# Optimization experiments

Hardware: AMD Instinct MI355X
Metric: run time of the kernel (lower is better)

Reference implementation:

```python
import jax, jax.numpy as jnp
import numpy as np

N = 100000     # graph nodes
D = 256        # input_dim
E = 1600000    # edges (avg degree 16)
S = 512        # sentences in the (single) doc
EMAX = 8       # max entities per sentence
H = 256        # lstm hidden_dim
ODIM = 1       # output_dim
NCONV = 2
EPS = 1e-6


def setup_inputs() -> dict:
    key = jax.random.key(0)
    ks = jax.random.split(key, 12)
    sc = 1.0 / np.sqrt(D)
    return {
        "x": jax.random.normal(ks[0], (N, D), jnp.float32),
        "edge_index": jax.random.randint(ks[1], (2, E), 0, N, jnp.int32),
        "entity_idx": jax.random.randint(ks[2], (S, EMAX), 0, N, jnp.int32),
        "entity_mask": jax.random.randint(ks[3], (S, EMAX), 0, 2, jnp.int32),
        "nsp_scores": jax.random.uniform(ks[4], (1, S - 1), jnp.float32),
        "cls_tokens": jax.random.normal(ks[5], (1, D), jnp.float32),
        "conv_W": jax.random.normal(ks[6], (NCONV, D, D), jnp.float32) * sc,
        "sent_W": jax.random.normal(ks[7], (D, D), jnp.float32) * sc,
        "sent_b": jnp.zeros((D,), jnp.float32),
        "W_ih": jax.random.normal(ks[8], (4 * H, D), jnp.float32) * sc,
        "W_hh": jax.random.normal(ks[9], (4 * H, H), jnp.float32) * sc,
        "b_ih": jnp.zeros((4 * H,), jnp.float32),
        "b_hh": jnp.zeros((4 * H,), jnp.float32),
        "red_W": jax.random.normal(ks[10], (256, D), jnp.float32) * sc,
        "red_b": jnp.zeros((256,), jnp.float32),
        "fin_W": jax.random.normal(ks[11], (ODIM, 512), jnp.float32) * (1.0 / np.sqrt(512.0)),
        "fin_b": jnp.full((ODIM,), 0.1, jnp.float32),
    }


def _forward(x, nsp_scores, cls_tokens, conv_W, sent_W, sent_b,
             W_ih, W_hh, b_ih, b_hh, red_W, red_b, fin_W, fin_b,
             edge_index, entity_idx, entity_mask):
    src, dst = edge_index[0], edge_index[1]
    # degree normalization: norm_e = deg[dst]^-1/2 * deg[src]^-1/2
    deg = jax.ops.segment_sum(jnp.ones((E,), x.dtype), dst, num_segments=N)
    dis = jnp.where(deg > 0, deg ** -0.5, jnp.zeros((), x.dtype))
    norm = dis[dst] * dis[src]                           # [E]
    h = x
    for i in range(NCONV):                               # GCN: transform, gather, weight, scatter-add
        msg = norm[:, None] * (h @ conv_W[i])[src]       # [E, D]
        h = jax.nn.relu(jax.ops.segment_sum(msg, dst, num_segments=N))
    # per-sentence entity gather -> linear+relu -> masked sum / (eps + count)
    ent = h[entity_idx]                                  # [S, EMAX, D]
    mask = entity_mask.astype(h.dtype)                   # [S, EMAX]
    lin = jax.nn.relu(ent @ sent_W.T + sent_b)           # [S, EMAX, D]
    sums = (lin * mask[..., None]).sum(axis=1)           # [S, D]
    lengths = mask.sum(axis=1)                           # [S]
    sent_feat = sums / (EPS + lengths)[:, None]          # [S, D]
    # single-layer unidirectional LSTM over sentences (batch = 1 doc); pytorch gate order i,f,g,o
    def step(carry, xt):
        h_t, c_t = carry
        gates = xt @ W_ih.T + b_ih + h_t @ W_hh.T + b_hh  # [1, 4H]
        i_, f_, g_, o_ = jnp.split(gates, 4, axis=-1)
        c = jax.nn.sigmoid(f_) * c_t + jax.nn.sigmoid(i_) * jnp.tanh(g_)
        hn = jax.nn.sigmoid(o_) * jnp.tanh(c)
        return (hn, c), hn
    h0 = jnp.zeros((1, H), x.dtype)
    c0 = jnp.zeros((1, H), x.dtype)
    _, outs = jax.lax.scan(step, (h0, c0), sent_feat[:, None, :])  # outs: [S, 1, H]
    output = jnp.swapaxes(outs, 0, 1)                    # [1, S, H]
    # NSP-score-weighted sum over adjacent lstm outputs
    sol = (nsp_scores[..., None] * (output[:, :-1] + output[:, 1:])).sum(axis=1)  # [1, H]
    red = cls_tokens[0] @ red_W.T + red_b                # [256]
    comb = jnp.concatenate([sol[0], red], axis=0)        # [512]
    out = comb @ fin_W.T + fin_b                         # [ODIM]
    return jax.nn.sigmoid(jax.nn.relu(out))


def reference(x, edge_index, entity_idx, entity_mask, nsp_scores, cls_tokens,
              conv_W, sent_W, sent_b, W_ih, W_hh, b_ih, b_hh,
              red_W, red_b, fin_W, fin_b):
    return _forward(x, nsp_scores, cls_tokens, conv_W, sent_W, sent_b,
                    W_ih, W_hh, b_ih, b_hh, red_W, red_b, fin_W, fin_b,
                    edge_index, entity_idx, entity_mask)
```

## Files before the change

kernel.cpp:

```cpp
#include <hip/hip_runtime.h>
#include <hip/hip_fp16.h>
#include <stdint.h>

constexpr int N    = 100000;
constexpr int D    = 256;
constexpr int E    = 1600000;
constexpr int S    = 512;
constexpr int EMAX = 8;
constexpr int H    = 256;
constexpr int G4   = 4 * H;
constexpr int NB   = (N + 255) / 256;

typedef _Float16 h2_t __attribute__((ext_vector_type(2)));
typedef __attribute__((ext_vector_type(8))) short short8;
typedef __attribute__((ext_vector_type(4))) float f32x4;

static __device__ __forceinline__ float fdot2f(uint32_t a, uint32_t b, float c) {
#if __has_builtin(__builtin_amdgcn_fdot2)
    return __builtin_amdgcn_fdot2(__builtin_bit_cast(h2_t, a), __builtin_bit_cast(h2_t, b), c, false);
#else
    __half2 ha = __builtin_bit_cast(__half2, a), hb = __builtin_bit_cast(__half2, b);
    float2 fa = __half22float2(ha), fb = __half22float2(hb);
    return c + fa.x * fb.x + fa.y * fb.y;
#endif
}

static __device__ __forceinline__ uint32_t bf16rne(float f) {
    uint32_t u = __builtin_bit_cast(uint32_t, f);
    return (u + 0x7FFFu + ((u >> 16) & 1u)) >> 16;
}
static __device__ __forceinline__ uint32_t pk2(float a, float b) {
    return bf16rne(a) | (bf16rne(b) << 16);
}
static __device__ __forceinline__ float bf2f(uint32_t hi16) {
    return __builtin_bit_cast(float, hi16 << 16);
}
static __device__ __forceinline__ float sigm(float x) { return 1.f / (1.f + __expf(-x)); }
static __device__ __forceinline__ float tanhfast(float x) {
    float e = __expf(-2.f * x);
    return 2.f / (1.f + e) - 1.f;
}

__global__ void k_deg(const int* __restrict__ dst, int* __restrict__ deg) {
    int e = blockIdx.x * 256 + threadIdx.x;
    if (e < E) atomicAdd(&deg[dst[e]], 1);
}

__global__ void k_dis(const int* __restrict__ deg, float* __restrict__ dis) {
    int n = blockIdx.x * 256 + threadIdx.x;
    if (n < N) {
        int d = deg[n];
        dis[n] = (d > 0) ? (1.0f / sqrtf((float)d)) : 0.0f;
    }
}

__global__ void k_scan1(const int* __restrict__ deg, int* __restrict__ bsum) {
    __shared__ int s[256];
    int i = blockIdx.x * 256 + threadIdx.x;
    s[threadIdx.x] = (i < N) ? deg[i] : 0;
    __syncthreads();
    for (int off = 128; off > 0; off >>= 1) {
        if (threadIdx.x < off) s[threadIdx.x] += s[threadIdx.x + off];
        __syncthreads();
    }
    if (threadIdx.x == 0) bsum[blockIdx.x] = s[0];
}

__global__ void k_scan2(const int* __restrict__ bsum, int* __restrict__ boff, int* __restrict__ row_ptr) {
    __shared__ int s[512];
    int t = threadIdx.x;
    int v = (t < NB) ? bsum[t] : 0;
    s[t] = v;
    __syncthreads();
    for (int off = 1; off < 512; off <<= 1) {
        int u = (t >= off) ? s[t - off] : 0;
        __syncthreads();
        s[t] += u;
        __syncthreads();
    }
    if (t < NB) boff[t] = s[t] - v;
    if (t == NB - 1) row_ptr[N] = s[t];
}

__global__ void k_scan3(const int* __restrict__ deg, const int* __restrict__ boff, int* __restrict__ row_ptr) {
    __shared__ int s[256];
    int t = threadIdx.x, i = blockIdx.x * 256 + t;
    int v = (i < N) ? deg[i] : 0;
    s[t] = v;
    __syncthreads();
    for (int off = 1; off < 256; off <<= 1) {
        int u = (t >= off) ? s[t - off] : 0;
        __syncthreads();
        s[t] += u;
        __syncthreads();
    }
    if (i < N) row_ptr[i] = boff[blockIdx.x] + s[t] - v;
}

__global__ void k_fill(const int* __restrict__ src, const int* __restrict__ dst,
                       const float* __restrict__ dis, const int* __restrict__ row_ptr,
                       int* __restrict__ cnt, int* __restrict__ col, float* __restrict__ ew) {
    int e = blockIdx.x * 256 + threadIdx.x;
    if (e < E) {
        int s_ = src[e], d_ = dst[e];
        float w = dis[d_] * dis[s_];
        int p = row_ptr[d_] + atomicAdd(&cnt[d_], 1);
        col[p] = s_;
        ew[p]  = w;
    }
}

__global__ void k_cvtB(const float* __restrict__ W, ushort* __restrict__ Bt) {
    int i = blockIdx.x * 256 + threadIdx.x;
    if (i < 2 * 256 * 256) {
        int L = i >> 16, n = (i >> 8) & 255, k = i & 255;
        Bt[i] = (ushort)bf16rne(W[L * 65536 + k * 256 + n]);
    }
}

template<bool AF32>
__global__ __launch_bounds__(512) void k_mmb(const void* __restrict__ Av, const ushort* __restrict__ Bt,
                                             ushort* __restrict__ Cb, int M) {
    __shared__ ushort As[128 * 32];
    __shared__ ushort Bs[256 * 32];
    const float*  Af = (const float*)Av;
    const ushort* Ah = (const ushort*)Av;
    int tid = threadIdx.x;
    int lane = tid & 63;
    int wid = tid >> 6, wr = wid >> 2, wc = wid & 3;
    int m0 = blockIdx.x * 128;
    int ra = tid >> 2, ca = tid & 3;

    f32x4 acc[4][4];
#pragma unroll
    for (int mi = 0; mi < 4; mi++)
#pragma unroll
        for (int ni = 0; ni < 4; ni++) acc[mi][ni] = (f32x4){0.f, 0.f, 0.f, 0.f};

    auto ldA = [&](int kt) -> uint4 {
        uint4 r{0u, 0u, 0u, 0u};
        int grow = m0 + ra;
        if (grow < M) {
            if constexpr (AF32) {
                const float* ap = Af + (size_t)grow * 256 + kt * 32 + ca * 8;
                float4 f0 = *(const float4*)ap;
                float4 f1 = *(const float4*)(ap + 4);
                r.x = pk2(f0.x, f0.y); r.y = pk2(f0.z, f0.w);
                r.z = pk2(f1.x, f1.y); r.w = pk2(f1.z, f1.w);
            } else {
                r = *(const uint4*)(Ah + (size_t)grow * 256 + kt * 32 + ca * 8);
            }
        }
        return r;
    };

    uint4 pa  = ldA(0);
    uint4 pb0 = *(const uint4*)&Bt[(size_t)ra * 256 + ca * 8];
    uint4 pb1 = *(const uint4*)&Bt[(size_t)(ra + 128) * 256 + ca * 8];

    for (int kt = 0; kt < 8; kt++) {
        *(uint4*)&As[ra * 32 + ca * 8] = pa;
        *(uint4*)&Bs[ra * 32 + ca * 8] = pb0;
        *(uint4*)&Bs[(ra + 128) * 32 + ca * 8] = pb1;
        __syncthreads();
        if (kt < 7) {
            pa  = ldA(kt + 1);
            pb0 = *(const uint4*)&Bt[(size_t)ra * 256 + (kt + 1) * 32 + ca * 8];
            pb1 = *(const uint4*)&Bt[(size_t)(ra + 128) * 256 + (kt + 1) * 32 + ca * 8];
        }
        short8 af[4], bf[4];
#pragma unroll
        for (int mi = 0; mi < 4; mi++)
            af[mi] = __builtin_bit_cast(short8,
                *(const uint4*)&As[(wr * 64 + mi * 16 + (lane & 15)) * 32 + (lane >> 4) * 8]);
#pragma unroll
        for (int ni = 0; ni < 4; ni++)
            bf[ni] = __builtin_bit_cast(short8,
                *(const uint4*)&Bs[(wc * 64 + ni * 16 + (lane & 15)) * 32 + (lane >> 4) * 8]);
#pragma unroll
        for (int mi = 0; mi < 4; mi++)
#pragma unroll
            for (int ni = 0; ni < 4; ni++)
                acc[mi][ni] = __builtin_amdgcn_mfma_f32_16x16x32_bf16(af[mi], bf[ni], acc[mi][ni], 0, 0, 0);
        __syncthreads();
    }

#pragma unroll
    for (int mi = 0; mi < 4; mi++)
#pragma unroll
        for (int j = 0; j < 4; j++) {
            int row = m0 + wr * 64 + mi * 16 + (lane >> 4) * 4 + j;
            if (row < M) {
#pragma unroll
                for (int ni = 0; ni < 4; ni++) {
                    int colc = wc * 64 + ni * 16 + (lane & 15);
                    Cb[(size_t)row * 256 + colc] = (ushort)bf16rne(acc[mi][ni][j]);
                }
            }
        }
}

__global__ __launch_bounds__(256) void k_aggb(const ushort* __restrict__ tb, const int* __restrict__ row_ptr,
                                              const int* __restrict__ col, const float* __restrict__ ew,
                                              ushort* __restrict__ ob) {
    int wid = blockIdx.x * 4 + (threadIdx.x >> 6);
    int lane = threadIdx.x & 63;
    if (wid >= N) return;
    int beg = row_ptr[wid], end = row_ptr[wid + 1];
    float a0 = 0.f, a1 = 0.f, a2 = 0.f, a3 = 0.f;
    int e = beg;
    for (; e + 4 <= end; e += 4) {
        int s0 = col[e], s1 = col[e + 1], s2 = col[e + 2], s3 = col[e + 3];
        float w0 = ew[e], w1 = ew[e + 1], w2 = ew[e + 2], w3 = ew[e + 3];
        ushort4 v0 = *(const ushort4*)&tb[(size_t)s0 * 256 + lane * 4];
        ushort4 v1 = *(const ushort4*)&tb[(size_t)s1 * 256 + lane * 4];
        ushort4 v2 = *(const ushort4*)&tb[(size_t)s2 * 256 + lane * 4];
        ushort4 v3 = *(const ushort4*)&tb[(size_t)s3 * 256 + lane * 4];
        a0 += w0 * bf2f(v0.x) + w1 * bf2f(v1.x) + w2 * bf2f(v2.x) + w3 * bf2f(v3.x);
        a1 += w0 * bf2f(v0.y) + w1 * bf2f(v1.y) + w2 * bf2f(v2.y) + w3 * bf2f(v3.y);
        a2 += w0 * bf2f(v0.z) + w1 * bf2f(v1.z) + w2 * bf2f(v2.z) + w3 * bf2f(v3.z);
        a3 += w0 * bf2f(v0.w) + w1 * bf2f(v1.w) + w2 * bf2f(v2.w) + w3 * bf2f(v3.w);
    }
    for (; e < end; e++) {
        int s0 = col[e];
        float w0 = ew[e];
        ushort4 v0 = *(const ushort4*)&tb[(size_t)s0 * 256 + lane * 4];
        a0 += w0 * bf2f(v0.x);
        a1 += w0 * bf2f(v0.y);
        a2 += w0 * bf2f(v0.z);
        a3 += w0 * bf2f(v0.w);
    }
    a0 = fmaxf(a0, 0.f); a1 = fmaxf(a1, 0.f); a2 = fmaxf(a2, 0.f); a3 = fmaxf(a3, 0.f);
    ushort4 o = {(ushort)bf16rne(a0), (ushort)bf16rne(a1), (ushort)bf16rne(a2), (ushort)bf16rne(a3)};
    *(ushort4*)&ob[(size_t)wid * 256 + lane * 4] = o;
}

__global__ __launch_bounds__(256) void k_sent3(const ushort* __restrict__ tb, const int* __restrict__ rowp,
                                               const int* __restrict__ col, const float* __restrict__ ew,
                                               const int* __restrict__ eidx, const int* __restrict__ emask,
                                               const float* __restrict__ sW, const float* __restrict__ sb,
                                               float* __restrict__ sf) {
    __shared__ float entS[8][256];
    int s_ = blockIdx.x, tid = threadIdx.x;
#pragma unroll
    for (int e = 0; e < EMAX; e++) {
        int mk = emask[s_ * EMAX + e];
        float acc = 0.f;
        if (mk) {
            int idx = eidx[s_ * EMAX + e];
            int beg = rowp[idx], end = rowp[idx + 1];
            int ed = beg;
            for (; ed + 2 <= end; ed += 2) {
                int n0 = col[ed], n1 = col[ed + 1];
                float w0 = ew[ed], w1 = ew[ed + 1];
                acc += w0 * bf2f(tb[(size_t)n0 * 256 + tid])
                     + w1 * bf2f(tb[(size_t)n1 * 256 + tid]);
            }
            if (ed < end) {
                acc += ew[ed] * bf2f(tb[(size_t)col[ed] * 256 + tid]);
            }
        }
        entS[e][tid] = fmaxf(acc, 0.f);
    }
    __syncthreads();
    float b = sb[tid];
    float acc[8];
#pragma unroll
    for (int e = 0; e < EMAX; e++) acc[e] = b;
    for (int k4 = 0; k4 < 64; k4++) {
        float4 w = *(const float4*)&sW[(size_t)tid * 256 + k4 * 4];
#pragma unroll
        for (int e = 0; e < EMAX; e++) {
            float4 v = *(const float4*)&entS[e][k4 * 4];
            acc[e] += w.x * v.x + w.y * v.y + w.z * v.z + w.w * v.w;
        }
    }
    float sum = 0.f, len = 0.f;
#pragma unroll
    for (int e = 0; e < EMAX; e++) {
        int mk = emask[s_ * EMAX + e];
        if (mk) { sum += fmaxf(acc[e], 0.f); len += 1.f; }
    }
    sf[(size_t)s_ * 256 + tid] = sum / (1e-6f + len);
}

__global__ __launch_bounds__(256) void k_xg2(const float* __restrict__ sf, const float* __restrict__ Wih,
                                             const float* __restrict__ bih, const float* __restrict__ bhh,
                                             float* __restrict__ Xg4) {
    __shared__ float sfS[16 * 256];
    int sb = blockIdx.x, y = blockIdx.y, tid = threadIdx.x;
    for (int i = tid; i < 16 * 256; i += 256) sfS[i] = sf[(size_t)(sb * 16) * 256 + i];
    __syncthreads();
    int r = y * 256 + tid;
    float acc[16];
#pragma unroll
    for (int si = 0; si < 16; si++) acc[si] = 0.f;
    for (int k4 = 0; k4 < 64; k4++) {
        float4 w = *(const float4*)&Wih[(size_t)r * 256 + k4 * 4];
#pragma unroll
        for (int si = 0; si < 16; si++) {
            float4 v = *(const float4*)&sfS[si * 256 + k4 * 4];
            acc[si] += w.x * v.x + w.y * v.y + w.z * v.z + w.w * v.w;
        }
    }
    float bb = bih[r] + bhh[r];
#pragma unroll
    for (int si = 0; si < 16; si++)
        Xg4[(size_t)(sb * 16 + si) * 1024 + tid * 4 + y] = acc[si] + bb;
}

__global__ void k_pack(const float* __restrict__ W, uint32_t* __restrict__ Wpk) {
    int idx = blockIdx.x * 256 + threadIdx.x;
    if (idx >= 2 * 64 * 1024) return;
    int p    = idx >> 16;
    int j4   = (idx >> 12) & 15;
    int tid  = (idx >> 2) & 1023;
    int m    = idx & 3;
    int j    = j4 * 4 + m;
    int gate = (p == 0) ? ((j < 32) ? 0 : 1) : ((j < 32) ? 2 : 3);
    int jj   = j & 31;
    int q    = tid >> 8, hidx = tid & 255;
    int row  = gate * 256 + hidx;
    int c0   = q * 64 + jj * 2;
    float a = W[row * 256 + c0], b = W[row * 256 + c0 + 1];
    uint32_t lo = (uint32_t)__half_as_ushort(__float2half(a));
    uint32_t hi = (uint32_t)__half_as_ushort(__float2half(b));
    Wpk[idx] = lo | (hi << 16);
}

__global__ __launch_bounds__(1024, 4) void k_lstm4(const float* __restrict__ Xg4,
                                                   const uint32_t* __restrict__ Wpk,
                                                   const float* __restrict__ nsp,
                                                   float* __restrict__ sol_out) {
    __shared__ uint32_t gW[32768];
    __shared__ uint32_t hqd[128];
    __shared__ float4   gsm4[1024];
    __shared__ float    nspS[512];
    int tid = threadIdx.x;
    int q = tid >> 8;
    const uint4* Wpk4 = (const uint4*)Wpk;
    uint4* gW4 = (uint4*)gW;

    uint4 wr[16];
#pragma unroll
    for (int j4 = 0; j4 < 16; j4++) wr[j4] = Wpk4[j4 * 1024 + tid];
#pragma unroll
    for (int k = 0; k < 8; k++) gW4[k * 1024 + tid] = Wpk4[16384 + k * 1024 + tid];

    if (tid < 128) hqd[tid] = 0u;
    if (tid < 512) nspS[tid] = (tid < 511) ? nsp[tid] : 0.f;
    float c = 0.f, sol = 0.f;
    __syncthreads();

    for (int t = 0; t < S; t++) {
        float4 xg;
        if (tid < 256) xg = *(const float4*)&Xg4[t * 1024 + tid * 4];
        float pi = 0.f, pf = 0.f, pg = 0.f, po = 0.f;
#pragma unroll
        for (int k = 0; k < 8; k++) {
            uint4 so = Wpk4[16384 + (k + 8) * 1024 + tid];
            uint4 sg = gW4[k * 1024 + tid];
            uint4 hv = *(const uint4*)&hqd[q * 32 + k * 4];
            pi = fdot2f(wr[k].x, hv.x, pi);
            pi = fdot2f(wr[k].y, hv.y, pi);
            pi = fdot2f(wr[k].z, hv.z, pi);
            pi = fdot2f(wr[k].w, hv.w, pi);
            pf = fdot2f(wr[k + 8].x, hv.x, pf);
            pf = fdot2f(wr[k + 8].y, hv.y, pf);
            pf = fdot2f(wr[k + 8].z, hv.z, pf);
            pf = fdot2f(wr[k + 8].w, hv.w, pf);
            pg = fdot2f(sg.x, hv.x, pg);
            pg = fdot2f(sg.y, hv.y, pg);
            pg = fdot2f(sg.z, hv.z, pg);
            pg = fdot2f(sg.w, hv.w, pg);
            po = fdot2f(so.x, hv.x, po);
            po = fdot2f(so.y, hv.y, po);
            po = fdot2f(so.z, hv.z, po);
            po = fdot2f(so.w, hv.w, po);
        }
        float4 part = {pi, pf, pg, po};
        gsm4[tid] = part;
        __syncthreads();
        if (tid < 256) {
            float gi = xg.x, gf = xg.y, gg = xg.z, go = xg.w;
#pragma unroll
            for (int qq = 0; qq < 4; qq++) {
                float4 v = gsm4[qq * 256 + tid];
                gi += v.x; gf += v.y; gg += v.z; go += v.w;
            }
            float i_ = sigm(gi);
            float f_ = sigm(gf);
            float g_ = tanhfast(gg);
            float o_ = sigm(go);
            c = f_ * c + i_ * g_;
            float h = o_ * tanhfast(c);
            float wgt = ((t > 0) ? nspS[t - 1] : 0.f) + nspS[t];
            sol += wgt * h;
            ((__half*)hqd)[tid] = __float2half(h);
        }
        __syncthreads();
    }
    if (tid < 256) sol_out[tid] = sol;
}

__global__ __launch_bounds__(256) void k_final(const float* __restrict__ sol, const float* __restrict__ cls,
                                               const float* __restrict__ redW, const float* __restrict__ redb,
                                               const float* __restrict__ finW, const float* __restrict__ finb,
                                               float* __restrict__ out) {
    __shared__ float clsS[256];
    __shared__ float psum[256];
    int j = threadIdx.x;
    clsS[j] = cls[j];
    __syncthreads();
    float acc = redb[j];
#pragma unroll 8
    for (int k = 0; k < 256; k++) acc += clsS[k] * redW[j * 256 + k];
    float p = sol[j] * finW[j] + acc * finW[256 + j];
    psum[j] = p;
    __syncthreads();
    for (int off = 128; off > 0; off >>= 1) {
        if (j < off) psum[j] += psum[j + off];
        __syncthreads();
    }
    if (j == 0) {
        float o = psum[0] + finb[0];
        o = fmaxf(o, 0.f);
        out[0] = 1.f / (1.f + expf(-o));
    }
}

extern "C" void kernel_launch(void* const* d_in, const int* in_sizes, int n_in,
                              void* d_out, int out_size, void* d_ws, size_t ws_size,
                              hipStream_t stream) {
    const float* x      = (const float*)d_in[0];
    const int*   eidx2  = (const int*)d_in[1];
    const int*   entidx = (const int*)d_in[2];
    const int*   entmsk = (const int*)d_in[3];
    const float* nsp    = (const float*)d_in[4];
    const float* cls    = (const float*)d_in[5];
    const float* convW  = (const float*)d_in[6];
    const float* sentW  = (const float*)d_in[7];
    const float* sentb  = (const float*)d_in[8];
    const float* Wih    = (const float*)d_in[9];
    const float* Whh    = (const float*)d_in[10];
    const float* bih    = (const float*)d_in[11];
    const float* bhh    = (const float*)d_in[12];
    const float* redW   = (const float*)d_in[13];
    const float* redb   = (const float*)d_in[14];
    const float* finW   = (const float*)d_in[15];
    const float* finb   = (const float*)d_in[16];
    const int* src = eidx2;
    const int* dst = eidx2 + E;

    char* w = (char*)d_ws;
    auto alloc = [&](size_t bytes) { char* p = w; w += (bytes + 255) & ~(size_t)255; return p; };
    int*      deg  = (int*)alloc((size_t)N * 4);
    float*    dis  = (float*)alloc((size_t)N * 4);
    int*      rowp = (int*)alloc((size_t)(N + 1) * 4);
    int*      cnt  = (int*)alloc((size_t)N * 4);
    int*      bsum = (int*)alloc((size_t)NB * 4);
    int*      boff = (int*)alloc((size_t)NB * 4);
    int*      col  = (int*)alloc((size_t)E * 4);
    float*    ew   = (float*)alloc((size_t)E * 4);
    ushort*   tb   = (ushort*)alloc((size_t)N * D * 2);
    ushort*   hb1  = (ushort*)alloc((size_t)N * D * 2);
    float*    sf   = (float*)alloc((size_t)S * D * 4);
    float*    Xg   = (float*)alloc((size_t)S * G4 * 4);
    uint32_t* Wpk  = (uint32_t*)alloc((size_t)2 * 64 * 1024 * 4);
    ushort*   Bt   = (ushort*)alloc((size_t)2 * 256 * 256 * 2);
    float*    sol  = (float*)alloc((size_t)H * 4);

    hipMemsetAsync(deg, 0, (size_t)N * 4, stream);
    hipMemsetAsync(cnt, 0, (size_t)N * 4, stream);

    k_deg<<<(E + 255) / 256, 256, 0, stream>>>(dst, deg);
    k_dis<<<(N + 255) / 256, 256, 0, stream>>>(deg, dis);
    k_scan1<<<NB, 256, 0, stream>>>(deg, bsum);
    k_scan2<<<1, 512, 0, stream>>>(bsum, boff, rowp);
    k_scan3<<<NB, 256, 0, stream>>>(deg, boff, rowp);
    k_fill<<<(E + 255) / 256, 256, 0, stream>>>(src, dst, dis, rowp, cnt, col, ew);
    k_pack<<<(2 * 64 * 1024 + 255) / 256, 256, 0, stream>>>(Whh, Wpk);
    k_cvtB<<<(2 * 256 * 256 + 255) / 256, 256, 0, stream>>>(convW, Bt);

    int mmg = (N + 127) / 128;
    k_mmb<true><<<mmg, 512, 0, stream>>>(x, Bt, tb, N);
    k_aggb<<<(N + 3) / 4, 256, 0, stream>>>(tb, rowp, col, ew, hb1);
    k_mmb<false><<<mmg, 512, 0, stream>>>(hb1, Bt + 65536, tb, N);

    k_sent3<<<S, 256, 0, stream>>>(tb, rowp, col, ew, entidx, entmsk, sentW, sentb, sf);
    k_xg2<<<dim3(32, 4), 256, 0, stream>>>(sf, Wih, bih, bhh, Xg);
    k_lstm4<<<1, 1024, 0, stream>>>(Xg, Wpk, nsp, sol);
    k_final<<<1, 256, 0, stream>>>(sol, cls, redW, redb, finW, finb, (float*)d_out);
}
```

Measured before the change: 1.200 ms.

## Reduce LSTM gate partials with DPP shuffles and double-buffer hidden state

Remaps the recurrent weight packing so the four K-quarter partials for each hidden unit sit in adjacent lanes. They are then summed with DPP xor-1/xor-2 moves instead of going through shared memory. The hidden state is double-buffered and padded, which removes one of the two block barriers per timestep in the sequential 512-step LSTM. In exchange, only one lane in four does the activation math, and the padded indexing must match the new packing layout.

```diff
diff --git a/kernel.cpp b/kernel.cpp
--- a/kernel.cpp
+++ b/kernel.cpp
@@ -39,6 +39,15 @@
 static __device__ __forceinline__ float tanhfast(float x) {
     float e = __expf(-2.f * x);
     return 2.f / (1.f + e) - 1.f;
+}
+
+static __device__ __forceinline__ float dpp_xor1_add(float x) {
+    int y = __builtin_amdgcn_mov_dpp(__builtin_bit_cast(int, x), 0xB1, 0xF, 0xF, true);
+    return x + __builtin_bit_cast(float, y);
+}
+static __device__ __forceinline__ float dpp_xor2_add(float x) {
+    int y = __builtin_amdgcn_mov_dpp(__builtin_bit_cast(int, x), 0x4E, 0xF, 0xF, true);
+    return x + __builtin_bit_cast(float, y);
 }
 
 __global__ void k_deg(const int* __restrict__ dst, int* __restrict__ deg) {
@@ -309,7 +318,7 @@
         Xg4[(size_t)(sb * 16 + si) * 1024 + tid * 4 + y] = acc[si] + bb;
 }
 
-__global__ void k_pack(const float* __restrict__ W, uint32_t* __restrict__ Wpk) {
+__global__ void k_pack2(const float* __restrict__ W, uint32_t* __restrict__ Wpk) {
     int idx = blockIdx.x * 256 + threadIdx.x;
     if (idx >= 2 * 64 * 1024) return;
     int p    = idx >> 16;
@@ -319,7 +328,8 @@
     int j    = j4 * 4 + m;
     int gate = (p == 0) ? ((j < 32) ? 0 : 1) : ((j < 32) ? 2 : 3);
     int jj   = j & 31;
-    int q    = tid >> 8, hidx = tid & 255;
+    int q    = tid & 3;
+    int hidx = ((tid >> 6) << 4) + ((tid >> 2) & 15);
     int row  = gate * 256 + hidx;
     int c0   = q * 64 + jj * 2;
     float a = W[row * 256 + c0], b = W[row * 256 + c0 + 1];
@@ -328,16 +338,18 @@
     Wpk[idx] = lo | (hi << 16);
 }
 
-__global__ __launch_bounds__(1024, 4) void k_lstm4(const float* __restrict__ Xg4,
+__global__ __launch_bounds__(1024, 4) void k_lstm7(const float* __restrict__ Xg4,
                                                    const uint32_t* __restrict__ Wpk,
                                                    const float* __restrict__ nsp,
                                                    float* __restrict__ sol_out) {
     __shared__ uint32_t gW[32768];
-    __shared__ uint32_t hqd[128];
-    __shared__ float4   gsm4[1024];
+    __shared__ uint32_t hqd[2][144];
     __shared__ float    nspS[512];
     int tid = threadIdx.x;
-    int q = tid >> 8;
+    int lane = tid & 63;
+    int q = lane & 3;
+    int hidx = ((tid >> 6) << 4) + (lane >> 2);
+    bool upd = (q == 0);
     const uint4* Wpk4 = (const uint4*)Wpk;
     uint4* gW4 = (uint4*)gW;
 
@@ -347,20 +359,21 @@
 #pragma unroll
     for (int k = 0; k < 8; k++) gW4[k * 1024 + tid] = Wpk4[16384 + k * 1024 + tid];
 
-    if (tid < 128) hqd[tid] = 0u;
+    if (tid < 288) ((uint32_t*)hqd)[tid] = 0u;
     if (tid < 512) nspS[tid] = (tid < 511) ? nsp[tid] : 0.f;
     float c = 0.f, sol = 0.f;
     __syncthreads();
 
     for (int t = 0; t < S; t++) {
+        const uint32_t* hb = hqd[t & 1];
         float4 xg;
-        if (tid < 256) xg = *(const float4*)&Xg4[t * 1024 + tid * 4];
+        if (upd) xg = *(const float4*)&Xg4[t * 1024 + hidx * 4];
         float pi = 0.f, pf = 0.f, pg = 0.f, po = 0.f;
 #pragma unroll
         for (int k = 0; k < 8; k++) {
             uint4 so = Wpk4[16384 + (k + 8) * 1024 + tid];
             uint4 sg = gW4[k * 1024 + tid];
-            uint4 hv = *(const uint4*)&hqd[q * 32 + k * 4];
+            uint4 hv = *(const uint4*)&hb[q * 36 + k * 4];
             pi = fdot2f(wr[k].x, hv.x, pi);
             pi = fdot2f(wr[k].y, hv.y, pi);
             pi = fdot2f(wr[k].z, hv.z, pi);
@@ -378,16 +391,12 @@
             po = fdot2f(so.z, hv.z, po);
             po = fdot2f(so.w, hv.w, po);
         }
-        float4 part = {pi, pf, pg, po};
-        gsm4[tid] = part;
-        __syncthreads();
-        if (tid < 256) {
-            float gi = xg.x, gf = xg.y, gg = xg.z, go = xg.w;
-#pragma unroll
-            for (int qq = 0; qq < 4; qq++) {
-                float4 v = gsm4[qq * 256 + tid];
-                gi += v.x; gf += v.y; gg += v.z; go += v.w;
-            }
+        pi = dpp_xor2_add(dpp_xor1_add(pi));
+        pf = dpp_xor2_add(dpp_xor1_add(pf));
+        pg = dpp_xor2_add(dpp_xor1_add(pg));
+        po = dpp_xor2_add(dpp_xor1_add(po));
+        if (upd) {
+            float gi = xg.x + pi, gf = xg.y + pf, gg = xg.z + pg, go = xg.w + po;
             float i_ = sigm(gi);
             float f_ = sigm(gf);
             float g_ = tanhfast(gg);
@@ -396,11 +405,11 @@
             float h = o_ * tanhfast(c);
             float wgt = ((t > 0) ? nspS[t - 1] : 0.f) + nspS[t];
             sol += wgt * h;
-            ((__half*)hqd)[tid] = __float2half(h);
-        }
-        __syncthreads();
-    }
-    if (tid < 256) sol_out[tid] = sol;
+            ((__half*)hqd[(t + 1) & 1])[(hidx >> 6) * 72 + (hidx & 63)] = __float2half(h);
+        }
+        __syncthreads();
+    }
+    if (upd) sol_out[hidx] = sol;
 }
 
 __global__ __launch_bounds__(256) void k_final(const float* __restrict__ sol, const float* __restrict__ cls,
@@ -479,7 +488,7 @@
     k_scan2<<<1, 512, 0, stream>>>(bsum, boff, rowp);
     k_scan3<<<NB, 256, 0, stream>>>(deg, boff, rowp);
     k_fill<<<(E + 255) / 256, 256, 0, stream>>>(src, dst, dis, rowp, cnt, col, ew);
-    k_pack<<<(2 * 64 * 1024 + 255) / 256, 256, 0, stream>>>(Whh, Wpk);
+    k_pack2<<<(2 * 64 * 1024 + 255) / 256, 256, 0, stream>>>(Whh, Wpk);
     k_cvtB<<<(2 * 256 * 256 + 255) / 256, 256, 0, stream>>>(convW, Bt);
 
     int mmg = (N + 127) / 128;
@@ -489,6 +498,6 @@
 
     k_sent3<<<S, 256, 0, stream>>>(tb, rowp, col, ew, entidx, entmsk, sentW, sentb, sf);
     k_xg2<<<dim3(32, 4), 256, 0, stream>>>(sf, Wih, bih, bhh, Xg);
-    k_lstm4<<<1, 1024, 0, stream>>>(Xg, Wpk, nsp, sol);
+    k_lstm7<<<1, 1024, 0, stream>>>(Xg, Wpk, nsp, sol);
     k_final<<<1, 256, 0, stream>>>(sol, cls, redW, redb, finW, finb, (float*)d_out);
 }
```

Measured after the change: 1.425 ms. 18.7% more time.
